# Performance work log

Measured on AMD Instinct MI355X. Metric: run time of the kernel, lower is better.

## Reference

```python
import jax, jax.numpy as jnp
import numpy as np

SEQ_LEN, N_VARS, N_SKILLS, D_IN = 120, 9, 32, 1
BATCH = 32768


def setup_inputs() -> dict:
    key = jax.random.key(0)
    ks = jax.random.split(key, 8)
    H, D = N_SKILLS, D_IN
    s = 1.0 / np.sqrt(H)  # torch LSTMCell init scale
    return {
        "x": jax.random.normal(ks[0], (BATCH, N_VARS * SEQ_LEN), dtype=jnp.float32),
        # nn.LSTMCell params (gate order i,f,g,o)
        "W_ih": jax.random.uniform(ks[1], (4 * H, D), jnp.float32, -s, s),
        "W_hh": jax.random.uniform(ks[2], (4 * H, H), jnp.float32, -s, s),
        "b_ih": jax.random.uniform(ks[3], (4 * H,), jnp.float32, -s, s),
        "b_hh": jax.random.uniform(ks[4], (4 * H,), jnp.float32, -s, s),
        # contextual gate params: cg_w Linear(D,H,bias=False), cg_u Linear(H,H)
        "cg_w": jax.random.uniform(ks[5], (H, D), jnp.float32, -s, s),
        "cg_u": jax.random.uniform(ks[6], (H, H), jnp.float32, -s, s),
        "cg_b": jax.random.uniform(ks[7], (H,), jnp.float32, -s, s),
    }


def reference(x, W_ih, W_hh, b_ih, b_hh, cg_w, cg_u, cg_b):
    B = x.shape[0]
    H = N_SKILLS
    # [B, V*T] -> fold the 9 independent variable-sequences into the batch dim
    # (the same cell weights are shared across vars), then scan over time.
    xs = x.reshape(B * N_VARS, SEQ_LEN, D_IN)
    xs = jnp.moveaxis(xs, 1, 0)  # [T, B*V, D_IN]

    def step(carry, xt):
        h, c = carry  # each [B*V, H]
        gates = xt @ W_ih.T + b_ih + h @ W_hh.T + b_hh  # [B*V, 4H]
        i, f, g, o = jnp.split(gates, 4, axis=-1)
        i = jax.nn.sigmoid(i)
        f = jax.nn.sigmoid(f)
        g = jnp.tanh(g)
        c_new = f * c + i * g
        # contextual gate uses the *previous* h
        cg = jax.nn.sigmoid(xt @ cg_w.T + h @ cg_u.T + cg_b)
        h_new = cg * jnp.tanh(c_new)
        return (h_new, c_new), None

    zeros = jnp.zeros((B * N_VARS, H), dtype=x.dtype)
    (h, _), _ = jax.lax.scan(step, (zeros, zeros), xs)
    # [B*V, H] -> [B, V*H] (variable-major, matching torch.cat over vars)
    return h.reshape(B, N_VARS * H)
```

## Files before the change

### kernel.cpp

```cpp
#include <hip/hip_runtime.h>


#define NV 9
#define TLEN 120
#define HS 32
#define BATCH_ 32768
#define NSEQ (BATCH_ * NV)
#define NBATCH (NSEQ / 16)
#define WPB 4
#define GRID_ (NBATCH / WPB)

#define TCHUNK 60
#define XSTRIDE 20
#define HSTRIDE 36

#define LOG2E 1.4426950408889634f
#define TWOL  2.8853900817779268f

typedef __attribute__((ext_vector_type(8))) short bf16x8;
typedef __attribute__((ext_vector_type(4))) float f32x4;
typedef __attribute__((ext_vector_type(4))) unsigned int u32x4;

__device__ __forceinline__ float fast_exp2(float x) { return __builtin_amdgcn_exp2f(x); }
__device__ __forceinline__ float fast_rcp(float x)  { return __builtin_amdgcn_rcpf(x); }
__device__ __forceinline__ unsigned int fbits(float x) { return __builtin_bit_cast(unsigned int, x); }
__device__ __forceinline__ float bcastf(unsigned int x) { return __builtin_bit_cast(float, x); }

__device__ __forceinline__ f32x4 splat4(float x) { f32x4 v = {x, x, x, x}; return v; }
__device__ __forceinline__ f32x4 fma4(f32x4 a, f32x4 b, f32x4 c) {
  return __builtin_elementwise_fma(a, b, c);
}
__device__ __forceinline__ f32x4 exp24(f32x4 v) {
  f32x4 r;
  r[0] = fast_exp2(v[0]); r[1] = fast_exp2(v[1]);
  r[2] = fast_exp2(v[2]); r[3] = fast_exp2(v[3]);
  return r;
}
__device__ __forceinline__ f32x4 rcp4(f32x4 v) {
  f32x4 r;
  r[0] = fast_rcp(v[0]); r[1] = fast_rcp(v[1]);
  r[2] = fast_rcp(v[2]); r[3] = fast_rcp(v[3]);
  return r;
}

__device__ __forceinline__ void lstm_elem(f32x4 ai, f32x4 af, f32x4 ag, f32x4 ac,
                                          f32x4& ct, f32x4& h) {
  const f32x4 one4 = splat4(1.0f);
  f32x4 Ei = exp24(ai), Ef = exp24(af), Eg = exp24(ag), Ea = exp24(ac);
  f32x4 pi_ = Ei + one4, pf_ = Ef + one4, pg_ = Eg + one4, pa_ = Ea + one4;
  f32x4 u   = fma4(Eg, splat4(TWOL), splat4(-TWOL));
  f32x4 P   = pi_ * pg_;
  f32x4 tt  = pf_ * u;
  f32x4 num = fma4(ct, P, tt);
  f32x4 den = pf_ * P;
  ct = num * rcp4(den);
  f32x4 Ec  = exp24(ct);
  h = (one4 - Ec) * rcp4(pa_ * (Ec + one4));
}

__global__ __launch_bounds__(256, 2) void cglstm_kernel(
    const float* __restrict__ x,
    const float* __restrict__ W_ih,
    const float* __restrict__ W_hh,
    const float* __restrict__ b_ih,
    const float* __restrict__ b_hh,
    const float* __restrict__ cg_w,
    const float* __restrict__ cg_u,
    const float* __restrict__ cg_b,
    float* __restrict__ out)
{
  const int lane = threadIdx.x & 63;
  const int wid  = threadIdx.x >> 6;
  const int col  = lane & 15;
  const int quad = lane >> 4;

  __shared__ __align__(16) float xT[WPB][TCHUNK * XSTRIDE];
  __shared__ unsigned int hbuf[WPB][16 * HSTRIDE];
  float* __restrict__ xTw = xT[wid];
  unsigned int* hb = hbuf[wid];

  bf16x8 bhi[8], blo[8];
  float wx[8], bb[8];
#pragma unroll
  for (int tile = 0; tile < 8; ++tile) {
    const int n = col + (tile & 1) * 16;
    const float sc_ = ((tile >> 1) == 2) ? -TWOL : -LOG2E;
    const float* wrow = (tile < 6) ? (W_hh + (size_t)((tile >> 1) * HS + n) * HS)
                                   : (cg_u + (size_t)n * HS);
    bf16x8 vh, vl;
#pragma unroll
    for (int e = 0; e < 8; ++e) {
      float wv = wrow[quad * 8 + e] * sc_;
      unsigned int wbits = fbits(wv);
      float lo_f = wv - bcastf(wbits & 0xffff0000u);
      vh[e] = (short)(wbits >> 16);
      vl[e] = (short)(fbits(lo_f) >> 16);
    }
    bhi[tile] = vh; blo[tile] = vl;
    if (tile < 6) {
      const int gg = tile >> 1;
      wx[tile] = W_ih[gg * HS + n] * sc_;
      bb[tile] = (b_ih[gg * HS + n] + b_hh[gg * HS + n]) * sc_;
    } else {
      wx[tile] = cg_w[n] * sc_;
      bb[tile] = cg_b[n] * sc_;
    }
  }

  const int p = blockIdx.x * WPB + wid;
  const float4* xb = (const float4*)(x + (size_t)p * 16 * TLEN);

  for (int i = lane; i < 16 * HSTRIDE; i += 64) hb[i] = 0u;
  f32x4 ct0 = splat4(0.f), ct1 = splat4(0.f), h0 = splat4(0.f), h1 = splat4(0.f);

#pragma unroll 1
  for (int chunk = 0; chunk < 2; ++chunk) {
    for (int i = lane; i < 240; i += 64) {
      int s = i / 15;
      int j = i - s * 15;
      float4 v = xb[s * 30 + chunk * 15 + j];
      int t0 = j * 4;
      xTw[(t0 + 0) * XSTRIDE + s] = v.x;
      xTw[(t0 + 1) * XSTRIDE + s] = v.y;
      xTw[(t0 + 2) * XSTRIDE + s] = v.z;
      xTw[(t0 + 3) * XSTRIDE + s] = v.w;
    }

#pragma unroll 1
    for (int tl = 0; tl < TCHUNK; ++tl) {
      f32x4 xt4 = *(const f32x4*)&xTw[tl * XSTRIDE + quad * 4];
      f32x4 acc[8];
#pragma unroll
      for (int tile = 0; tile < 8; ++tile)
        acc[tile] = fma4(splat4(wx[tile]), xt4, splat4(bb[tile]));
      const unsigned int* hrow = &hb[col * HSTRIDE + quad * 8];
      u32x4 wa = *(const u32x4*)hrow;
      u32x4 wz = *(const u32x4*)(hrow + 4);
      u32x4 hi4, lo4;
      hi4[0] = __builtin_amdgcn_perm(wa[1], wa[0], 0x05040100u);
      hi4[1] = __builtin_amdgcn_perm(wa[3], wa[2], 0x05040100u);
      hi4[2] = __builtin_amdgcn_perm(wz[1], wz[0], 0x05040100u);
      hi4[3] = __builtin_amdgcn_perm(wz[3], wz[2], 0x05040100u);
      lo4[0] = __builtin_amdgcn_perm(wa[1], wa[0], 0x07060302u);
      lo4[1] = __builtin_amdgcn_perm(wa[3], wa[2], 0x07060302u);
      lo4[2] = __builtin_amdgcn_perm(wz[1], wz[0], 0x07060302u);
      lo4[3] = __builtin_amdgcn_perm(wz[3], wz[2], 0x07060302u);
      bf16x8 ahi = __builtin_bit_cast(bf16x8, hi4);
      bf16x8 alo = __builtin_bit_cast(bf16x8, lo4);
#pragma unroll
      for (int tile = 0; tile < 8; ++tile) {
        acc[tile] = __builtin_amdgcn_mfma_f32_16x16x32_bf16(ahi, bhi[tile], acc[tile], 0, 0, 0);
        acc[tile] = __builtin_amdgcn_mfma_f32_16x16x32_bf16(alo, bhi[tile], acc[tile], 0, 0, 0);
        acc[tile] = __builtin_amdgcn_mfma_f32_16x16x32_bf16(ahi, blo[tile], acc[tile], 0, 0, 0);
      }
      lstm_elem(acc[0], acc[2], acc[4], acc[6], ct0, h0);
      lstm_elem(acc[1], acc[3], acc[5], acc[7], ct1, h1);
#pragma unroll
      for (int r = 0; r < 4; ++r) {
        unsigned int hbits = fbits(h0[r]);
        float lof = h0[r] - bcastf(hbits & 0xffff0000u);
        hb[(quad * 4 + r) * HSTRIDE + col] =
            __builtin_amdgcn_perm(fbits(lof), hbits, 0x07060302u);
        unsigned int hbits1 = fbits(h1[r]);
        float lof1 = h1[r] - bcastf(hbits1 & 0xffff0000u);
        hb[(quad * 4 + r) * HSTRIDE + col + 16] =
            __builtin_amdgcn_perm(fbits(lof1), hbits1, 0x07060302u);
      }
    }
  }

  float* ob = out + (size_t)p * 16 * HS;
#pragma unroll
  for (int r = 0; r < 4; ++r) {
    ob[(quad * 4 + r) * HS + col]      = h0[r];
    ob[(quad * 4 + r) * HS + col + 16] = h1[r];
  }
}

extern "C" void kernel_launch(void* const* d_in, const int* in_sizes, int n_in,
                              void* d_out, int out_size, void* d_ws, size_t ws_size,
                              hipStream_t stream) {
  const float* x    = (const float*)d_in[0];
  const float* W_ih = (const float*)d_in[1];
  const float* W_hh = (const float*)d_in[2];
  const float* b_ih = (const float*)d_in[3];
  const float* b_hh = (const float*)d_in[4];
  const float* cg_w = (const float*)d_in[5];
  const float* cg_u = (const float*)d_in[6];
  const float* cg_b = (const float*)d_in[7];
  float* out = (float*)d_out;

  dim3 grid(GRID_), block(256);
  hipLaunchKernelGGL(cglstm_kernel, grid, block, 0, stream,
                     x, W_ih, W_hh, b_ih, b_hh, cg_w, cg_u, cg_b, out);
}
```

Measured before the change: 1.381 ms.

## Interleave two independent 16-sequence batches per wave to hide recurrence latency

Each wave now processes two independent groups of 16 sequences and interleaves their per-step work. The MFMA chains of one group can overlap with the transcendental elementwise math of the other. This hides the serial dependency latency of the recurrent step. In exchange the grid is halved, register pressure roughly doubles for accumulators and state, and LDS use per block doubles, which may reduce occupancy under launch_bounds(256,2).

```diff
diff --git a/kernel.cpp b/kernel.cpp
--- a/kernel.cpp
+++ b/kernel.cpp
@@ -8,7 +8,7 @@
 #define NSEQ (BATCH_ * NV)
 #define NBATCH (NSEQ / 16)
 #define WPB 4
-#define GRID_ (NBATCH / WPB)
+#define GRID_ (NBATCH / (WPB * 2))
 
 #define TCHUNK 60
 #define XSTRIDE 20
@@ -56,6 +56,56 @@
   ct = num * rcp4(den);
   f32x4 Ec  = exp24(ct);
   h = (one4 - Ec) * rcp4(pa_ * (Ec + one4));
+}
+
+__device__ __forceinline__ void gates8(const unsigned int* __restrict__ hb,
+                                       const float* __restrict__ xTw, int tl,
+                                       int col, int quad,
+                                       const bf16x8 (&bhi)[8], const bf16x8 (&blo)[8],
+                                       const float (&wx)[8], const float (&bb)[8],
+                                       f32x4 (&acc)[8]) {
+  f32x4 xt4 = *(const f32x4*)&xTw[tl * XSTRIDE + quad * 4];
+#pragma unroll
+  for (int tile = 0; tile < 8; ++tile)
+    acc[tile] = fma4(splat4(wx[tile]), xt4, splat4(bb[tile]));
+  const unsigned int* hrow = &hb[col * HSTRIDE + quad * 8];
+  u32x4 wa = *(const u32x4*)hrow;
+  u32x4 wz = *(const u32x4*)(hrow + 4);
+  u32x4 hi4, lo4;
+  hi4[0] = __builtin_amdgcn_perm(wa[1], wa[0], 0x05040100u);
+  hi4[1] = __builtin_amdgcn_perm(wa[3], wa[2], 0x05040100u);
+  hi4[2] = __builtin_amdgcn_perm(wz[1], wz[0], 0x05040100u);
+  hi4[3] = __builtin_amdgcn_perm(wz[3], wz[2], 0x05040100u);
+  lo4[0] = __builtin_amdgcn_perm(wa[1], wa[0], 0x07060302u);
+  lo4[1] = __builtin_amdgcn_perm(wa[3], wa[2], 0x07060302u);
+  lo4[2] = __builtin_amdgcn_perm(wz[1], wz[0], 0x07060302u);
+  lo4[3] = __builtin_amdgcn_perm(wz[3], wz[2], 0x07060302u);
+  bf16x8 ahi = __builtin_bit_cast(bf16x8, hi4);
+  bf16x8 alo = __builtin_bit_cast(bf16x8, lo4);
+#pragma unroll
+  for (int tile = 0; tile < 8; ++tile) {
+    acc[tile] = __builtin_amdgcn_mfma_f32_16x16x32_bf16(ahi, bhi[tile], acc[tile], 0, 0, 0);
+    acc[tile] = __builtin_amdgcn_mfma_f32_16x16x32_bf16(alo, bhi[tile], acc[tile], 0, 0, 0);
+    acc[tile] = __builtin_amdgcn_mfma_f32_16x16x32_bf16(ahi, blo[tile], acc[tile], 0, 0, 0);
+  }
+}
+
+__device__ __forceinline__ void finish8(unsigned int* __restrict__ hb, int col, int quad,
+                                        f32x4 (&acc)[8],
+                                        f32x4& ct0, f32x4& ct1, f32x4& h0, f32x4& h1) {
+  lstm_elem(acc[0], acc[2], acc[4], acc[6], ct0, h0);
+  lstm_elem(acc[1], acc[3], acc[5], acc[7], ct1, h1);
+#pragma unroll
+  for (int r = 0; r < 4; ++r) {
+    unsigned int hbits = fbits(h0[r]);
+    float lof = h0[r] - bcastf(hbits & 0xffff0000u);
+    hb[(quad * 4 + r) * HSTRIDE + col] =
+        __builtin_amdgcn_perm(fbits(lof), hbits, 0x07060302u);
+    unsigned int hbits1 = fbits(h1[r]);
+    float lof1 = h1[r] - bcastf(hbits1 & 0xffff0000u);
+    hb[(quad * 4 + r) * HSTRIDE + col + 16] =
+        __builtin_amdgcn_perm(fbits(lof1), hbits1, 0x07060302u);
+  }
 }
 
 __global__ __launch_bounds__(256, 2) void cglstm_kernel(
@@ -74,10 +124,12 @@
   const int col  = lane & 15;
   const int quad = lane >> 4;
 
-  __shared__ __align__(16) float xT[WPB][TCHUNK * XSTRIDE];
-  __shared__ unsigned int hbuf[WPB][16 * HSTRIDE];
-  float* __restrict__ xTw = xT[wid];
-  unsigned int* hb = hbuf[wid];
+  __shared__ __align__(16) float xT[WPB][2][TCHUNK * XSTRIDE];
+  __shared__ __align__(16) unsigned int hbuf[WPB][2][16 * HSTRIDE];
+  float* __restrict__ xTw0 = xT[wid][0];
+  float* __restrict__ xTw1 = xT[wid][1];
+  unsigned int* hb0 = hbuf[wid][0];
+  unsigned int* hb1 = hbuf[wid][1];
 
   bf16x8 bhi[8], blo[8];
   float wx[8], bb[8];
@@ -107,73 +159,56 @@
     }
   }
 
-  const int p = blockIdx.x * WPB + wid;
-  const float4* xb = (const float4*)(x + (size_t)p * 16 * TLEN);
-
-  for (int i = lane; i < 16 * HSTRIDE; i += 64) hb[i] = 0u;
-  f32x4 ct0 = splat4(0.f), ct1 = splat4(0.f), h0 = splat4(0.f), h1 = splat4(0.f);
+  const int p0 = (blockIdx.x * WPB + wid) * 2;
+  const int p1 = p0 + 1;
+  const float4* xb0 = (const float4*)(x + (size_t)p0 * 16 * TLEN);
+  const float4* xb1 = (const float4*)(x + (size_t)p1 * 16 * TLEN);
+
+  for (int i = lane; i < 2 * 16 * HSTRIDE; i += 64) hb0[i] = 0u;
+  f32x4 cA0 = splat4(0.f), cA1 = splat4(0.f), hA0 = splat4(0.f), hA1 = splat4(0.f);
+  f32x4 cB0 = splat4(0.f), cB1 = splat4(0.f), hB0 = splat4(0.f), hB1 = splat4(0.f);
 
 #pragma unroll 1
   for (int chunk = 0; chunk < 2; ++chunk) {
     for (int i = lane; i < 240; i += 64) {
       int s = i / 15;
       int j = i - s * 15;
-      float4 v = xb[s * 30 + chunk * 15 + j];
+      float4 v = xb0[s * 30 + chunk * 15 + j];
       int t0 = j * 4;
-      xTw[(t0 + 0) * XSTRIDE + s] = v.x;
-      xTw[(t0 + 1) * XSTRIDE + s] = v.y;
-      xTw[(t0 + 2) * XSTRIDE + s] = v.z;
-      xTw[(t0 + 3) * XSTRIDE + s] = v.w;
+      xTw0[(t0 + 0) * XSTRIDE + s] = v.x;
+      xTw0[(t0 + 1) * XSTRIDE + s] = v.y;
+      xTw0[(t0 + 2) * XSTRIDE + s] = v.z;
+      xTw0[(t0 + 3) * XSTRIDE + s] = v.w;
+    }
+    for (int i = lane; i < 240; i += 64) {
+      int s = i / 15;
+      int j = i - s * 15;
+      float4 v = xb1[s * 30 + chunk * 15 + j];
+      int t0 = j * 4;
+      xTw1[(t0 + 0) * XSTRIDE + s] = v.x;
+      xTw1[(t0 + 1) * XSTRIDE + s] = v.y;
+      xTw1[(t0 + 2) * XSTRIDE + s] = v.z;
+      xTw1[(t0 + 3) * XSTRIDE + s] = v.w;
     }
 
 #pragma unroll 1
     for (int tl = 0; tl < TCHUNK; ++tl) {
-      f32x4 xt4 = *(const f32x4*)&xTw[tl * XSTRIDE + quad * 4];
-      f32x4 acc[8];
-#pragma unroll
-      for (int tile = 0; tile < 8; ++tile)
-        acc[tile] = fma4(splat4(wx[tile]), xt4, splat4(bb[tile]));
-      const unsigned int* hrow = &hb[col * HSTRIDE + quad * 8];
-      u32x4 wa = *(const u32x4*)hrow;
-      u32x4 wz = *(const u32x4*)(hrow + 4);
-      u32x4 hi4, lo4;
-      hi4[0] = __builtin_amdgcn_perm(wa[1], wa[0], 0x05040100u);
-      hi4[1] = __builtin_amdgcn_perm(wa[3], wa[2], 0x05040100u);
-      hi4[2] = __builtin_amdgcn_perm(wz[1], wz[0], 0x05040100u);
-      hi4[3] = __builtin_amdgcn_perm(wz[3], wz[2], 0x05040100u);
-      lo4[0] = __builtin_amdgcn_perm(wa[1], wa[0], 0x07060302u);
-      lo4[1] = __builtin_amdgcn_perm(wa[3], wa[2], 0x07060302u);
-      lo4[2] = __builtin_amdgcn_perm(wz[1], wz[0], 0x07060302u);
-      lo4[3] = __builtin_amdgcn_perm(wz[3], wz[2], 0x07060302u);
-      bf16x8 ahi = __builtin_bit_cast(bf16x8, hi4);
-      bf16x8 alo = __builtin_bit_cast(bf16x8, lo4);
-#pragma unroll
-      for (int tile = 0; tile < 8; ++tile) {
-        acc[tile] = __builtin_amdgcn_mfma_f32_16x16x32_bf16(ahi, bhi[tile], acc[tile], 0, 0, 0);
-        acc[tile] = __builtin_amdgcn_mfma_f32_16x16x32_bf16(alo, bhi[tile], acc[tile], 0, 0, 0);
-        acc[tile] = __builtin_amdgcn_mfma_f32_16x16x32_bf16(ahi, blo[tile], acc[tile], 0, 0, 0);
-      }
-      lstm_elem(acc[0], acc[2], acc[4], acc[6], ct0, h0);
-      lstm_elem(acc[1], acc[3], acc[5], acc[7], ct1, h1);
-#pragma unroll
-      for (int r = 0; r < 4; ++r) {
-        unsigned int hbits = fbits(h0[r]);
-        float lof = h0[r] - bcastf(hbits & 0xffff0000u);
-        hb[(quad * 4 + r) * HSTRIDE + col] =
-            __builtin_amdgcn_perm(fbits(lof), hbits, 0x07060302u);
-        unsigned int hbits1 = fbits(h1[r]);
-        float lof1 = h1[r] - bcastf(hbits1 & 0xffff0000u);
-        hb[(quad * 4 + r) * HSTRIDE + col + 16] =
-            __builtin_amdgcn_perm(fbits(lof1), hbits1, 0x07060302u);
-      }
-    }
-  }
-
-  float* ob = out + (size_t)p * 16 * HS;
+      f32x4 acc0[8], acc1[8];
+      gates8(hb0, xTw0, tl, col, quad, bhi, blo, wx, bb, acc0);
+      gates8(hb1, xTw1, tl, col, quad, bhi, blo, wx, bb, acc1);
+      finish8(hb0, col, quad, acc0, cA0, cA1, hA0, hA1);
+      finish8(hb1, col, quad, acc1, cB0, cB1, hB0, hB1);
+    }
+  }
+
+  float* ob0 = out + (size_t)p0 * 16 * HS;
+  float* ob1 = out + (size_t)p1 * 16 * HS;
 #pragma unroll
   for (int r = 0; r < 4; ++r) {
-    ob[(quad * 4 + r) * HS + col]      = h0[r];
-    ob[(quad * 4 + r) * HS + col + 16] = h1[r];
+    ob0[(quad * 4 + r) * HS + col]      = hA0[r];
+    ob0[(quad * 4 + r) * HS + col + 16] = hA1[r];
+    ob1[(quad * 4 + r) * HS + col]      = hB0[r];
+    ob1[(quad * 4 + r) * HS + col + 16] = hB1[r];
   }
 }
 
```

Measured after the change: 1.370 ms. Within noise of the previous version (-0.8%).
